# Kernel optimization log

Hardware: AMD Instinct MI355X
Metric: run time of the kernel (lower is better)

## Reference

```python
import jax, jax.numpy as jnp
import numpy as np

N_NODES = 100000
N_EDGES = 1600000
HID = 64


def _gcn_conv(x, src, dst, W, b, n_nodes):
    """PyG GCNConv: add self-loops, symmetric deg normalization, linear transform.
    out_i = sum_{j in N(i) u {i}} deg_i^{-1/2} deg_j^{-1/2} (x_j W) + b
    """
    h = x @ W  # [N, out] small matmul
    loops = jnp.arange(n_nodes, dtype=src.dtype)
    s = jnp.concatenate([src, loops])  # sources (message senders)
    d = jnp.concatenate([dst, loops])  # targets (aggregation index)
    deg = jax.ops.segment_sum(jnp.ones_like(d, dtype=h.dtype), d, num_segments=n_nodes)
    dinv = jnp.where(deg > 0, jax.lax.rsqrt(deg), 0.0)
    coef = dinv[s] * dinv[d]  # [E+N]
    msg = h[s] * coef[:, None]  # gather + scale (memory-bound)
    out = jax.ops.segment_sum(msg, d, num_segments=n_nodes)  # scatter-add
    return out + b


def setup_inputs() -> dict:
    key = jax.random.key(0)
    ks = jax.random.split(key, 16)
    x = jax.random.normal(ks[0], (N_NODES, 4), dtype=jnp.float32)
    edge_index = jax.random.randint(ks[1], (2, N_EDGES), 0, N_NODES, dtype=jnp.int64)
    s = 0.1
    params = {
        'W1': jax.random.normal(ks[2], (4, HID), dtype=jnp.float32) * s,
        'b1': jnp.zeros((HID,), dtype=jnp.float32),
        'W2': jax.random.normal(ks[3], (HID, HID), dtype=jnp.float32) * s,
        'b2': jnp.zeros((HID,), dtype=jnp.float32),
        'W3': jax.random.normal(ks[4], (HID, HID), dtype=jnp.float32) * s,
        'b3': jnp.zeros((HID,), dtype=jnp.float32),
        'Wp': jax.random.normal(ks[5], (HID, HID), dtype=jnp.float32) * s,
        'bp': jnp.zeros((HID,), dtype=jnp.float32),
        'Wa': jax.random.normal(ks[6], (HID, 4), dtype=jnp.float32) * s,
        'ba': jnp.zeros((4,), dtype=jnp.float32),
        'Wm': jax.random.normal(ks[7], (HID, 2), dtype=jnp.float32) * s,
        'bm': jnp.zeros((2,), dtype=jnp.float32),
        'Wg': jax.random.normal(ks[8], (HID, 3), dtype=jnp.float32) * s,
        'bg': jnp.zeros((3,), dtype=jnp.float32),
        'Wt': jax.random.normal(ks[9], (HID, 10), dtype=jnp.float32) * s,
        'bt': jnp.zeros((10,), dtype=jnp.float32),
    }
    return {'x': x, 'edge_index': edge_index, 'node_index': 0, **params}


def reference(x, edge_index, node_index, W1, b1, W2, b2, W3, b3, Wp, bp, Wa, ba, Wm, bm, Wg, bg, Wt, bt):
    src, dst = edge_index[0], edge_index[1]
    n = x.shape[0]
    # dropout is identity in eval mode
    h = jax.nn.relu(_gcn_conv(x, src, dst, W1, b1, n))
    h = jax.nn.relu(_gcn_conv(h, src, dst, W2, b2, n))
    h = jax.nn.relu(_gcn_conv(h, src, dst, W3, b3, n))
    node = h[node_index]
    node = jax.nn.relu(node @ Wp + bp)
    return (node @ Wa + ba, node @ Wm + bm, node @ Wg + bg, node @ Wt + bt)
```

## Files before the change

### kernel.cpp

```cpp
#include <hip/hip_runtime.h>


#define HID  64
#define CAP1 2048
#define CAP2 512
#define RB1  128
#define RB2  128
#define CL3  2048
#define VE   8
#define TPB  256

__device__ __forceinline__ int detect64(const void* ei) {
  const unsigned* e32 = (const unsigned*)ei;
  int lane = threadIdx.x & 63;
  bool z = (e32[2 * lane + 1] == 0u);
  return (__ballot(z) == ~0ull) ? 1 : 0;
}

__device__ __forceinline__ int ld_src(const void* ei, int is64, long long e) {
  return is64 ? (int)((const unsigned*)ei)[e << 1] : ((const int*)ei)[e];
}

__device__ __forceinline__ int load_dsts(const void* ei, long long E, long long base,
                                         int is64, int d[VE]) {
  int n = (int)((E - base) < VE ? (E - base) : VE);
  if (is64) {
    const unsigned long long* p = (const unsigned long long*)ei + E + base;
    if (n == VE && (((E + base) & 1) == 0)) {
      const ulonglong2* q = (const ulonglong2*)p;
#pragma unroll
      for (int k = 0; k < VE / 2; ++k) {
        ulonglong2 v = q[k];
        d[2 * k] = (int)(unsigned)v.x; d[2 * k + 1] = (int)(unsigned)v.y;
      }
    } else {
      for (int k = 0; k < n; ++k) d[k] = (int)(unsigned)p[k];
    }
  } else {
    const int* p = (const int*)ei + E + base;
    if (n == VE && (((E + base) & 3) == 0)) {
      const int4* q = (const int4*)p;
#pragma unroll
      for (int k = 0; k < VE / 4; ++k) {
        int4 v = q[k];
        d[4 * k] = v.x; d[4 * k + 1] = v.y; d[4 * k + 2] = v.z; d[4 * k + 3] = v.w;
      }
    } else {
      for (int k = 0; k < n; ++k) d[k] = p[k];
    }
  }
  return n;
}

__device__ __forceinline__ int load_dsts32(const int* dst32, long long E,
                                           long long base, int d[VE]) {
  int n = (int)((E - base) < VE ? (E - base) : VE);
  if (n == VE) {
    int4 a = ((const int4*)(dst32 + base))[0];
    int4 b = ((const int4*)(dst32 + base))[1];
    d[0] = a.x; d[1] = a.y; d[2] = a.z; d[3] = a.w;
    d[4] = b.x; d[5] = b.y; d[6] = b.z; d[7] = b.w;
  } else {
    for (int k = 0; k < n; ++k) d[k] = dst32[base + k];
  }
  return n;
}

__global__ void k_scanF1(const void* ei, int E, const int* nidx_p, int* dst32,
                         int* slot2, int* node2, int* cnt2, int* l3, int* ec3) {
  int is64 = detect64(ei);
  int nidx = *nidx_p;
  if (blockIdx.x == 0 && threadIdx.x == 0) {
    if (atomicCAS(&slot2[nidx], 0, -1) == 0) {
      int p = atomicAdd(cnt2, 1) & (CAP2 - 1);
      slot2[nidx] = p + 1; node2[p] = nidx;
    }
  }
  long long base = ((long long)blockIdx.x * TPB + threadIdx.x) * VE;
  if (base >= E) return;
  int d[VE];
  int n = load_dsts(ei, E, base, is64, d);
  if (n == VE) {
    ((int4*)(dst32 + base))[0] = make_int4(d[0], d[1], d[2], d[3]);
    ((int4*)(dst32 + base))[1] = make_int4(d[4], d[5], d[6], d[7]);
  } else {
    for (int k = 0; k < n; ++k) dst32[base + k] = d[k];
  }
  for (int k = 0; k < n; ++k) {
    if (d[k] == nidx) {
      int s = ld_src(ei, is64, base + k);
      if (atomicCAS(&slot2[s], 0, -1) == 0) {
        int p = atomicAdd(cnt2, 1) & (CAP2 - 1);
        slot2[s] = p + 1; node2[p] = s;
      }
      int q = atomicAdd(ec3, 1);
      if (q < CL3) l3[q] = s;
    }
  }
}

__global__ void k_scanF2(const void* ei, int E, const int* dst32,
                         const int* slot2, const int* node2, const int* cnt2,
                         int* slot1, int* node1, int* need, int* cnt1,
                         int* rc2, int* bl2) {
  int rows2 = min(*cnt2, CAP2);
  for (int r = threadIdx.x; r < rows2; r += TPB) {
    int i = node2[r];
    need[i] = 1;
    if (atomicCAS(&slot1[i], 0, -1) == 0) {
      int p = atomicAdd(cnt1, 1) & (CAP1 - 1);
      slot1[i] = p + 1; node1[p] = i;
    }
  }
  int is64 = detect64(ei);
  long long base = ((long long)blockIdx.x * TPB + threadIdx.x) * VE;
  if (base >= E) return;
  int d[VE];
  int n = load_dsts32(dst32, E, base, d);
  for (int k = 0; k < n; ++k) {
    int sv = slot2[d[k]];
    if (sv > 0) {
      int ad = sv - 1;
      int s = ld_src(ei, is64, base + k);
      need[s] = 1;
      if (atomicCAS(&slot1[s], 0, -1) == 0) {
        int p = atomicAdd(cnt1, 1) & (CAP1 - 1);
        slot1[s] = p + 1; node1[p] = s;
      }
      int q = atomicAdd(&rc2[ad], 1);
      if (q < RB2) bl2[ad * RB2 + q] = s;
    }
  }
}

__global__ void k_scanS(const void* ei, int E, const int* dst32,
                        const int* slot1, int* need, int* rc1, int* bl1) {
  int is64 = detect64(ei);
  long long base = ((long long)blockIdx.x * TPB + threadIdx.x) * VE;
  if (base >= E) return;
  int d[VE];
  int n = load_dsts32(dst32, E, base, d);
  for (int k = 0; k < n; ++k) {
    int sv = slot1[d[k]];
    if (sv > 0) {
      int ad = sv - 1;
      int s = ld_src(ei, is64, base + k);
      need[s] = 1;
      int q = atomicAdd(&rc1[ad], 1);
      if (q < RB1) bl1[ad * RB1 + q] = s;
    }
  }
}

__global__ void k_scanDeg(int E, const int* dst32, const int* need, int* deg) {
  long long base = ((long long)blockIdx.x * TPB + threadIdx.x) * VE;
  if (base >= E) return;
  int d[VE];
  int n = load_dsts32(dst32, E, base, d);
  for (int k = 0; k < n; ++k)
    if (need[d[k]]) atomicAdd(&deg[d[k]], 1);
}

__global__ void k_l1(const float* __restrict__ x, const float* __restrict__ W1,
                     const float* __restrict__ b1, const int* __restrict__ deg,
                     const int* __restrict__ node1, const int* __restrict__ cnt1,
                     const int* __restrict__ rc1, const int* __restrict__ bl1,
                     float* __restrict__ h1c) {
  int w = blockIdx.x * 4 + (threadIdx.x >> 6);
  int lane = threadIdx.x & 63;
  int rows = min(*cnt1, CAP1);
  if (w >= rows) return;
  int i = node1[w];
  float di = 1.0f / sqrtf((float)(deg[i] + 1));
  int cnt = min(rc1[w], RB1);
  float ax = 0.f, ay = 0.f, az = 0.f, aw = 0.f;
  for (int j = lane; j < cnt; j += 64) {
    int s = bl1[w * RB1 + j];
    float c = (1.0f / sqrtf((float)(deg[s] + 1))) * di;
    float4 xv = ((const float4*)x)[s];
    ax += c * xv.x; ay += c * xv.y; az += c * xv.z; aw += c * xv.w;
  }
#pragma unroll
  for (int t = 1; t < 64; t <<= 1) {
    ax += __shfl_xor(ax, t); ay += __shfl_xor(ay, t);
    az += __shfl_xor(az, t); aw += __shfl_xor(aw, t);
  }
  float4 xi = ((const float4*)x)[i];
  float dd = di * di;
  ax += dd * xi.x; ay += dd * xi.y; az += dd * xi.z; aw += dd * xi.w;
  float v = ax * W1[lane] + ay * W1[64 + lane] + az * W1[128 + lane] +
            aw * W1[192 + lane] + b1[lane];
  h1c[w * HID + lane] = v > 0.f ? v : 0.f;
}

__global__ void k_l2(const float* __restrict__ W2, const float* __restrict__ b2,
                     const int* __restrict__ deg, const int* __restrict__ node2,
                     const int* __restrict__ cnt2, const int* __restrict__ slot1,
                     const int* __restrict__ rc2, const int* __restrict__ bl2,
                     const float* __restrict__ h1c, float* __restrict__ h2c) {
  __shared__ float sh[4][HID];
  int wv = threadIdx.x >> 6, lane = threadIdx.x & 63;
  int w = blockIdx.x * 4 + wv;
  int rows = min(*cnt2, CAP2);
  if (w >= rows) return;
  int i = node2[w];
  float di = 1.0f / sqrtf((float)(deg[i] + 1));
  int cnt = min(rc2[w], RB2);
  float acc = 0.f;
  for (int j0 = 0; j0 < cnt; j0 += 64) {
    int nb = min(64, cnt - j0);
    int sl = 0; float c = 0.f;
    if (lane < nb) {
      int s = bl2[w * RB2 + j0 + lane];
      sl = slot1[s] - 1;
      c = (1.0f / sqrtf((float)(deg[s] + 1))) * di;
    }
    int j = 0;
    for (; j + 8 <= nb; j += 8) {
      int r0 = __shfl(sl, j + 0), r1 = __shfl(sl, j + 1);
      int r2 = __shfl(sl, j + 2), r3 = __shfl(sl, j + 3);
      int r4 = __shfl(sl, j + 4), r5 = __shfl(sl, j + 5);
      int r6 = __shfl(sl, j + 6), r7 = __shfl(sl, j + 7);
      float v0 = h1c[r0 * HID + lane];
      float v1 = h1c[r1 * HID + lane];
      float v2 = h1c[r2 * HID + lane];
      float v3 = h1c[r3 * HID + lane];
      float v4 = h1c[r4 * HID + lane];
      float v5 = h1c[r5 * HID + lane];
      float v6 = h1c[r6 * HID + lane];
      float v7 = h1c[r7 * HID + lane];
      acc += __shfl(c, j + 0) * v0 + __shfl(c, j + 1) * v1 +
             __shfl(c, j + 2) * v2 + __shfl(c, j + 3) * v3 +
             __shfl(c, j + 4) * v4 + __shfl(c, j + 5) * v5 +
             __shfl(c, j + 6) * v6 + __shfl(c, j + 7) * v7;
    }
    for (; j < nb; ++j)
      acc += __shfl(c, j) * h1c[__shfl(sl, j) * HID + lane];
  }
  acc += di * di * h1c[(slot1[i] - 1) * HID + lane];
  sh[wv][lane] = acc;
  float v = b2[lane];
#pragma unroll 16
  for (int k = 0; k < HID; ++k) v += sh[wv][k] * W2[k * HID + lane];
  h2c[w * HID + lane] = v > 0.f ? v : 0.f;
}

__global__ void k_tail(const int* nidx_p, const int* slot2, const int* deg,
                       const float* h2c, const int* l3, const int* ec3,
                       const float* W3, const float* b3,
                       const float* Wp, const float* bp,
                       const float* Wa, const float* ba,
                       const float* Wm, const float* bm,
                       const float* Wg, const float* bg,
                       const float* Wt, const float* bt, float* out) {
  __shared__ float part[4][HID];
  __shared__ float g3[HID];
  __shared__ float h3[HID];
  __shared__ float p[HID];
  __shared__ int   ssl[64];
  __shared__ float scc[64];
  int tid = threadIdx.x, wv = tid >> 6, lane = tid & 63;
  int nidx = *nidx_p;
  float dn = 1.0f / sqrtf((float)(deg[nidx] + 1));
  int cnt = min(*ec3, CL3);
  float acc = 0.f;
  for (int j0 = 0; j0 < cnt; j0 += 64) {
    int nb = min(64, cnt - j0);
    if (tid < nb) {
      int s = l3[j0 + tid];
      ssl[tid] = slot2[s] - 1;
      scc[tid] = (1.0f / sqrtf((float)(deg[s] + 1))) * dn;
    }
    __syncthreads();
    int j = wv;
    for (; j + 12 < nb; j += 16) {
      int r0 = ssl[j], r1 = ssl[j + 4], r2 = ssl[j + 8], r3 = ssl[j + 12];
      float v0 = h2c[r0 * HID + lane];
      float v1 = h2c[r1 * HID + lane];
      float v2 = h2c[r2 * HID + lane];
      float v3 = h2c[r3 * HID + lane];
      acc += scc[j] * v0 + scc[j + 4] * v1 + scc[j + 8] * v2 + scc[j + 12] * v3;
    }
    for (; j < nb; j += 4)
      acc += scc[j] * h2c[ssl[j] * HID + lane];
    __syncthreads();
  }
  part[wv][lane] = acc;
  __syncthreads();
  if (wv == 0) {
    float a = part[0][lane] + part[1][lane] + part[2][lane] + part[3][lane];
    a += dn * dn * h2c[(slot2[nidx] - 1) * HID + lane];
    g3[lane] = a;
  }
  __syncthreads();
  {
    float v = 0.f;
    int k0 = wv * 16;
#pragma unroll 16
    for (int k = 0; k < 16; ++k) v += g3[k0 + k] * W3[(k0 + k) * HID + lane];
    part[wv][lane] = v;
  }
  __syncthreads();
  if (wv == 0) {
    float v = part[0][lane] + part[1][lane] + part[2][lane] + part[3][lane] +
              b3[lane];
    h3[lane] = v > 0.f ? v : 0.f;
  }
  __syncthreads();
  {
    float v = 0.f;
    int k0 = wv * 16;
#pragma unroll 16
    for (int k = 0; k < 16; ++k) v += h3[k0 + k] * Wp[(k0 + k) * HID + lane];
    part[wv][lane] = v;
  }
  __syncthreads();
  if (wv == 0) {
    float v = part[0][lane] + part[1][lane] + part[2][lane] + part[3][lane] +
              bp[lane];
    p[lane] = v > 0.f ? v : 0.f;
  }
  __syncthreads();
  if (tid < 4) {
    float o = ba[tid];
#pragma unroll 8
    for (int k = 0; k < HID; ++k) o += p[k] * Wa[k * 4 + tid];
    out[tid] = o;
  } else if (tid < 6) {
    int c = tid - 4; float o = bm[c];
#pragma unroll 8
    for (int k = 0; k < HID; ++k) o += p[k] * Wm[k * 2 + c];
    out[tid] = o;
  } else if (tid < 9) {
    int c = tid - 6; float o = bg[c];
#pragma unroll 8
    for (int k = 0; k < HID; ++k) o += p[k] * Wg[k * 3 + c];
    out[tid] = o;
  } else if (tid < 19) {
    int c = tid - 9; float o = bt[c];
#pragma unroll 8
    for (int k = 0; k < HID; ++k) o += p[k] * Wt[k * 10 + c];
    out[tid] = o;
  }
}

extern "C" void kernel_launch(void* const* d_in, const int* in_sizes, int n_in,
                              void* d_out, int out_size, void* d_ws, size_t ws_size,
                              hipStream_t stream) {
  const float* x  = (const float*)d_in[0];
  const void*  ei = d_in[1];
  const int* nidx = (const int*)d_in[2];
  const float* W1 = (const float*)d_in[3];
  const float* b1 = (const float*)d_in[4];
  const float* W2 = (const float*)d_in[5];
  const float* b2 = (const float*)d_in[6];
  const float* W3 = (const float*)d_in[7];
  const float* b3 = (const float*)d_in[8];
  const float* Wp = (const float*)d_in[9];
  const float* bp = (const float*)d_in[10];
  const float* Wa = (const float*)d_in[11];
  const float* ba = (const float*)d_in[12];
  const float* Wm = (const float*)d_in[13];
  const float* bm = (const float*)d_in[14];
  const float* Wg = (const float*)d_in[15];
  const float* bg = (const float*)d_in[16];
  const float* Wt = (const float*)d_in[17];
  const float* bt = (const float*)d_in[18];
  float* out = (float*)d_out;

  int N = in_sizes[0] / 4;
  int E = in_sizes[1] / 2;

  char* w = (char*)d_ws;
  size_t o = 0;
  auto take = [&](size_t bytes) -> void* {
    void* p = w + o;
    o += (bytes + 255) & ~(size_t)255;
    return p;
  };
  size_t zeroInts = (size_t)8 + 2 * (size_t)N + CAP1 + CAP2 + 2 * (size_t)N;
  int* zr = (int*)take(zeroInts * 4);
  int* cnt1  = zr + 0;
  int* cnt2  = zr + 1;
  int* ec3   = zr + 2;
  int* deg   = zr + 8;
  int* need  = deg + N;
  int* rc1   = need + N;
  int* rc2   = rc1 + CAP1;
  int* slot1 = rc2 + CAP2;
  int* slot2 = slot1 + N;
  int*   dst32 = (int*)take((size_t)E * 4);
  int*   node1 = (int*)take((size_t)CAP1 * 4);
  int*   node2 = (int*)take((size_t)CAP2 * 4);
  int*   bl1   = (int*)take((size_t)CAP1 * RB1 * 4);
  int*   bl2   = (int*)take((size_t)CAP2 * RB2 * 4);
  int*   l3    = (int*)take((size_t)CL3 * 4);
  float* h1c   = (float*)take((size_t)CAP1 * HID * 4);
  float* h2c   = (float*)take((size_t)CAP2 * HID * 4);

  int gS = (int)(((long long)E + TPB * VE - 1) / (TPB * VE));

  hipMemsetAsync(zr, 0x00, zeroInts * 4, stream);
  k_scanF1 <<<gS, TPB, 0, stream>>>(ei, E, nidx, dst32, slot2, node2, cnt2, l3, ec3);
  k_scanF2 <<<gS, TPB, 0, stream>>>(ei, E, dst32, slot2, node2, cnt2,
                                    slot1, node1, need, cnt1, rc2, bl2);
  k_scanS  <<<gS, TPB, 0, stream>>>(ei, E, dst32, slot1, need, rc1, bl1);
  k_scanDeg<<<gS, TPB, 0, stream>>>(E, dst32, need, deg);
  k_l1     <<<CAP1 / 4, TPB, 0, stream>>>(x, W1, b1, deg, node1, cnt1, rc1, bl1, h1c);
  k_l2     <<<CAP2 / 4, TPB, 0, stream>>>(W2, b2, deg, node2, cnt2, slot1, rc2, bl2, h1c, h2c);
  k_tail   <<<1, TPB, 0, stream>>>(nidx, slot2, deg, h2c, l3, ec3, W3, b3, Wp, bp,
                                   Wa, ba, Wm, bm, Wg, bg, Wt, bt, out);
}
```

Before: 170.2 us.

## Fuse layer-2 aggregation and tail into one 1024-thread block

Merges the layer-2 gather/transform kernel with the single-block tail kernel, so 16 waves first compute the needed layer-2 rows and then do the final aggregation and MLP heads. The first 64 layer-2 rows are kept in shared memory to avoid a global round trip. This removes one kernel launch and its dependency gap. The risk is that layer-2 work now runs on a single CU, which is slow if many 2-hop rows are needed.

```diff
diff --git a/kernel.cpp b/kernel.cpp
--- a/kernel.cpp
+++ b/kernel.cpp
@@ -9,6 +9,8 @@
 #define CL3  2048
 #define VE   8
 #define TPB  256
+#define TT   1024
+#define NW   16
 
 __device__ __forceinline__ int detect64(const void* ei) {
   const unsigned* e32 = (const unsigned*)ei;
@@ -193,67 +195,24 @@
   h1c[w * HID + lane] = v > 0.f ? v : 0.f;
 }
 
-__global__ void k_l2(const float* __restrict__ W2, const float* __restrict__ b2,
-                     const int* __restrict__ deg, const int* __restrict__ node2,
-                     const int* __restrict__ cnt2, const int* __restrict__ slot1,
-                     const int* __restrict__ rc2, const int* __restrict__ bl2,
-                     const float* __restrict__ h1c, float* __restrict__ h2c) {
-  __shared__ float sh[4][HID];
-  int wv = threadIdx.x >> 6, lane = threadIdx.x & 63;
-  int w = blockIdx.x * 4 + wv;
-  int rows = min(*cnt2, CAP2);
-  if (w >= rows) return;
-  int i = node2[w];
-  float di = 1.0f / sqrtf((float)(deg[i] + 1));
-  int cnt = min(rc2[w], RB2);
-  float acc = 0.f;
-  for (int j0 = 0; j0 < cnt; j0 += 64) {
-    int nb = min(64, cnt - j0);
-    int sl = 0; float c = 0.f;
-    if (lane < nb) {
-      int s = bl2[w * RB2 + j0 + lane];
-      sl = slot1[s] - 1;
-      c = (1.0f / sqrtf((float)(deg[s] + 1))) * di;
-    }
-    int j = 0;
-    for (; j + 8 <= nb; j += 8) {
-      int r0 = __shfl(sl, j + 0), r1 = __shfl(sl, j + 1);
-      int r2 = __shfl(sl, j + 2), r3 = __shfl(sl, j + 3);
-      int r4 = __shfl(sl, j + 4), r5 = __shfl(sl, j + 5);
-      int r6 = __shfl(sl, j + 6), r7 = __shfl(sl, j + 7);
-      float v0 = h1c[r0 * HID + lane];
-      float v1 = h1c[r1 * HID + lane];
-      float v2 = h1c[r2 * HID + lane];
-      float v3 = h1c[r3 * HID + lane];
-      float v4 = h1c[r4 * HID + lane];
-      float v5 = h1c[r5 * HID + lane];
-      float v6 = h1c[r6 * HID + lane];
-      float v7 = h1c[r7 * HID + lane];
-      acc += __shfl(c, j + 0) * v0 + __shfl(c, j + 1) * v1 +
-             __shfl(c, j + 2) * v2 + __shfl(c, j + 3) * v3 +
-             __shfl(c, j + 4) * v4 + __shfl(c, j + 5) * v5 +
-             __shfl(c, j + 6) * v6 + __shfl(c, j + 7) * v7;
-    }
-    for (; j < nb; ++j)
-      acc += __shfl(c, j) * h1c[__shfl(sl, j) * HID + lane];
-  }
-  acc += di * di * h1c[(slot1[i] - 1) * HID + lane];
-  sh[wv][lane] = acc;
-  float v = b2[lane];
-#pragma unroll 16
-  for (int k = 0; k < HID; ++k) v += sh[wv][k] * W2[k * HID + lane];
-  h2c[w * HID + lane] = v > 0.f ? v : 0.f;
-}
-
-__global__ void k_tail(const int* nidx_p, const int* slot2, const int* deg,
-                       const float* h2c, const int* l3, const int* ec3,
-                       const float* W3, const float* b3,
-                       const float* Wp, const float* bp,
-                       const float* Wa, const float* ba,
-                       const float* Wm, const float* bm,
-                       const float* Wg, const float* bg,
-                       const float* Wt, const float* bt, float* out) {
-  __shared__ float part[4][HID];
+__global__ __launch_bounds__(TT) void k_l2tail(
+    const float* __restrict__ W2, const float* __restrict__ b2,
+    const int* __restrict__ deg, const int* __restrict__ node2,
+    const int* __restrict__ cnt2, const int* __restrict__ slot1,
+    const int* __restrict__ rc2, const int* __restrict__ bl2,
+    const float* __restrict__ h1c, float* __restrict__ h2c,
+    const int* __restrict__ nidx_p, const int* __restrict__ slot2,
+    const int* __restrict__ l3, const int* __restrict__ ec3,
+    const float* __restrict__ W3, const float* __restrict__ b3,
+    const float* __restrict__ Wp, const float* __restrict__ bp,
+    const float* __restrict__ Wa, const float* __restrict__ ba,
+    const float* __restrict__ Wm, const float* __restrict__ bm,
+    const float* __restrict__ Wg, const float* __restrict__ bg,
+    const float* __restrict__ Wt, const float* __restrict__ bt,
+    float* __restrict__ out) {
+  __shared__ float h2s[64][HID];
+  __shared__ float sh[NW][HID];
+  __shared__ float part[NW][HID];
   __shared__ float g3[HID];
   __shared__ float h3[HID];
   __shared__ float p[HID];
@@ -261,6 +220,53 @@
   __shared__ float scc[64];
   int tid = threadIdx.x, wv = tid >> 6, lane = tid & 63;
   int nidx = *nidx_p;
+  int rows = min(*cnt2, CAP2);
+
+  for (int w = wv; w < rows; w += NW) {
+    int i = node2[w];
+    float di = 1.0f / sqrtf((float)(deg[i] + 1));
+    int cnt = min(rc2[w], RB2);
+    float acc = 0.f;
+    for (int j0 = 0; j0 < cnt; j0 += 64) {
+      int nb = min(64, cnt - j0);
+      int sl = 0; float c = 0.f;
+      if (lane < nb) {
+        int s = bl2[w * RB2 + j0 + lane];
+        sl = slot1[s] - 1;
+        c = (1.0f / sqrtf((float)(deg[s] + 1))) * di;
+      }
+      int j = 0;
+      for (; j + 8 <= nb; j += 8) {
+        int r0 = __shfl(sl, j + 0), r1 = __shfl(sl, j + 1);
+        int r2 = __shfl(sl, j + 2), r3 = __shfl(sl, j + 3);
+        int r4 = __shfl(sl, j + 4), r5 = __shfl(sl, j + 5);
+        int r6 = __shfl(sl, j + 6), r7 = __shfl(sl, j + 7);
+        float v0 = h1c[r0 * HID + lane];
+        float v1 = h1c[r1 * HID + lane];
+        float v2 = h1c[r2 * HID + lane];
+        float v3 = h1c[r3 * HID + lane];
+        float v4 = h1c[r4 * HID + lane];
+        float v5 = h1c[r5 * HID + lane];
+        float v6 = h1c[r6 * HID + lane];
+        float v7 = h1c[r7 * HID + lane];
+        acc += __shfl(c, j + 0) * v0 + __shfl(c, j + 1) * v1 +
+               __shfl(c, j + 2) * v2 + __shfl(c, j + 3) * v3 +
+               __shfl(c, j + 4) * v4 + __shfl(c, j + 5) * v5 +
+               __shfl(c, j + 6) * v6 + __shfl(c, j + 7) * v7;
+      }
+      for (; j < nb; ++j)
+        acc += __shfl(c, j) * h1c[__shfl(sl, j) * HID + lane];
+    }
+    acc += di * di * h1c[(slot1[i] - 1) * HID + lane];
+    sh[wv][lane] = acc;
+    float v = b2[lane];
+#pragma unroll 16
+    for (int k = 0; k < HID; ++k) v += sh[wv][k] * W2[k * HID + lane];
+    v = v > 0.f ? v : 0.f;
+    if (w < 64) h2s[w][lane] = v; else h2c[w * HID + lane] = v;
+  }
+  __syncthreads();
+
   float dn = 1.0f / sqrtf((float)(deg[nidx] + 1));
   int cnt = min(*ec3, CL3);
   float acc = 0.f;
@@ -273,51 +279,62 @@
     }
     __syncthreads();
     int j = wv;
-    for (; j + 12 < nb; j += 16) {
-      int r0 = ssl[j], r1 = ssl[j + 4], r2 = ssl[j + 8], r3 = ssl[j + 12];
-      float v0 = h2c[r0 * HID + lane];
-      float v1 = h2c[r1 * HID + lane];
-      float v2 = h2c[r2 * HID + lane];
-      float v3 = h2c[r3 * HID + lane];
-      acc += scc[j] * v0 + scc[j + 4] * v1 + scc[j + 8] * v2 + scc[j + 12] * v3;
-    }
-    for (; j < nb; j += 4)
-      acc += scc[j] * h2c[ssl[j] * HID + lane];
+    for (; j + 48 < nb; j += 64) {
+      int r0 = ssl[j], r1 = ssl[j + 16], r2 = ssl[j + 32], r3 = ssl[j + 48];
+      float v0 = (r0 < 64) ? h2s[r0][lane] : h2c[r0 * HID + lane];
+      float v1 = (r1 < 64) ? h2s[r1][lane] : h2c[r1 * HID + lane];
+      float v2 = (r2 < 64) ? h2s[r2][lane] : h2c[r2 * HID + lane];
+      float v3 = (r3 < 64) ? h2s[r3][lane] : h2c[r3 * HID + lane];
+      acc += scc[j] * v0 + scc[j + 16] * v1 + scc[j + 32] * v2 +
+             scc[j + 48] * v3;
+    }
+    for (; j < nb; j += NW) {
+      int r = ssl[j];
+      float hv = (r < 64) ? h2s[r][lane] : h2c[r * HID + lane];
+      acc += scc[j] * hv;
+    }
     __syncthreads();
   }
   part[wv][lane] = acc;
   __syncthreads();
   if (wv == 0) {
-    float a = part[0][lane] + part[1][lane] + part[2][lane] + part[3][lane];
-    a += dn * dn * h2c[(slot2[nidx] - 1) * HID + lane];
-    g3[lane] = a;
+    float a = 0.f;
+#pragma unroll
+    for (int u = 0; u < NW; ++u) a += part[u][lane];
+    int r = slot2[nidx] - 1;
+    float hv = (r < 64) ? h2s[r][lane] : h2c[r * HID + lane];
+    g3[lane] = a + dn * dn * hv;
   }
   __syncthreads();
   {
-    float v = 0.f;
-    int k0 = wv * 16;
-#pragma unroll 16
-    for (int k = 0; k < 16; ++k) v += g3[k0 + k] * W3[(k0 + k) * HID + lane];
+    int k0 = wv * 4;
+    float v = g3[k0] * W3[k0 * HID + lane] +
+              g3[k0 + 1] * W3[(k0 + 1) * HID + lane] +
+              g3[k0 + 2] * W3[(k0 + 2) * HID + lane] +
+              g3[k0 + 3] * W3[(k0 + 3) * HID + lane];
     part[wv][lane] = v;
   }
   __syncthreads();
   if (wv == 0) {
-    float v = part[0][lane] + part[1][lane] + part[2][lane] + part[3][lane] +
-              b3[lane];
+    float v = b3[lane];
+#pragma unroll
+    for (int u = 0; u < NW; ++u) v += part[u][lane];
     h3[lane] = v > 0.f ? v : 0.f;
   }
   __syncthreads();
   {
-    float v = 0.f;
-    int k0 = wv * 16;
-#pragma unroll 16
-    for (int k = 0; k < 16; ++k) v += h3[k0 + k] * Wp[(k0 + k) * HID + lane];
+    int k0 = wv * 4;
+    float v = h3[k0] * Wp[k0 * HID + lane] +
+              h3[k0 + 1] * Wp[(k0 + 1) * HID + lane] +
+              h3[k0 + 2] * Wp[(k0 + 2) * HID + lane] +
+              h3[k0 + 3] * Wp[(k0 + 3) * HID + lane];
     part[wv][lane] = v;
   }
   __syncthreads();
   if (wv == 0) {
-    float v = part[0][lane] + part[1][lane] + part[2][lane] + part[3][lane] +
-              bp[lane];
+    float v = bp[lane];
+#pragma unroll
+    for (int u = 0; u < NW; ++u) v += part[u][lane];
     p[lane] = v > 0.f ? v : 0.f;
   }
   __syncthreads();
@@ -407,7 +424,7 @@
   k_scanS  <<<gS, TPB, 0, stream>>>(ei, E, dst32, slot1, need, rc1, bl1);
   k_scanDeg<<<gS, TPB, 0, stream>>>(E, dst32, need, deg);
   k_l1     <<<CAP1 / 4, TPB, 0, stream>>>(x, W1, b1, deg, node1, cnt1, rc1, bl1, h1c);
-  k_l2     <<<CAP2 / 4, TPB, 0, stream>>>(W2, b2, deg, node2, cnt2, slot1, rc2, bl2, h1c, h2c);
-  k_tail   <<<1, TPB, 0, stream>>>(nidx, slot2, deg, h2c, l3, ec3, W3, b3, Wp, bp,
-                                   Wa, ba, Wm, bm, Wg, bg, Wt, bt, out);
-}
+  k_l2tail <<<1, TT, 0, stream>>>(W2, b2, deg, node2, cnt2, slot1, rc2, bl2,
+                                  h1c, h2c, nidx, slot2, l3, ec3, W3, b3,
+                                  Wp, bp, Wa, ba, Wm, bm, Wg, bg, Wt, bt, out);
+}
```

Result: no change. 169.2 us (-0.6%).
